# Optimization experiments

Hardware: AMD Instinct MI355X
Metric: run time of the kernel (lower is better)

The kernel has to match this reference:

```python
import jax, jax.numpy as jnp
import numpy as np

J = 21      # joints
C_ENC = 256 # encoding channels
C_IMG = 512 # img_feat channels
D = 64      # depth bins (hard-coded by view(-1, 256, 64))
EPS = 1e-5


def _soft_argmax_1d(h):
    # h: [B, J, L]
    p = jax.nn.softmax(h, axis=2)
    pos = jnp.arange(h.shape[2], dtype=h.dtype)
    return jnp.sum(p * pos, axis=2, keepdims=True)  # [B, J, 1]


def setup_inputs() -> dict:
    key = jax.random.key(0)
    ks = jax.random.split(key, 12)
    B, H, W = 16, 16, 16
    img_feat = jax.random.normal(ks[0], (B, C_IMG, H, W), dtype=jnp.float32)
    encoding = jax.random.normal(ks[1], (B, C_ENC, H, W), dtype=jnp.float32)
    # 1x1 conv weights stored as [out, in]
    wx = jax.random.normal(ks[2], (J, C_ENC), dtype=jnp.float32) * 0.02
    bx = jnp.zeros((J,), dtype=jnp.float32)
    wy = jax.random.normal(ks[3], (J, C_ENC), dtype=jnp.float32) * 0.02
    by = jnp.zeros((J,), dtype=jnp.float32)
    wz1 = jax.random.normal(ks[4], (C_ENC * D, C_IMG), dtype=jnp.float32) * 0.02
    bz1 = jnp.zeros((C_ENC * D,), dtype=jnp.float32)
    gamma = jax.random.uniform(ks[5], (C_ENC * D,), dtype=jnp.float32, minval=0.5, maxval=1.5)
    beta = jax.random.normal(ks[6], (C_ENC * D,), dtype=jnp.float32) * 0.1
    rmean = jax.random.normal(ks[7], (C_ENC * D,), dtype=jnp.float32) * 0.1
    rvar = jax.random.uniform(ks[8], (C_ENC * D,), dtype=jnp.float32, minval=0.5, maxval=1.5)
    wz2 = jax.random.normal(ks[9], (J, C_ENC), dtype=jnp.float32) * 0.02
    bz2 = jnp.zeros((J,), dtype=jnp.float32)
    return {"img_feat": img_feat, "encoding": encoding,
            "wx": wx, "bx": bx, "wy": wy, "by": by,
            "wz1": wz1, "bz1": bz1, "gamma": gamma, "beta": beta,
            "rmean": rmean, "rvar": rvar, "wz2": wz2, "bz2": bz2}


def reference(img_feat, encoding, wx, bx, wy, by, wz1, bz1, gamma, beta, rmean, rvar, wz2, bz2):
    B = encoding.shape[0]
    # x branch: mean over H (dim 2) -> [B, 256, W]
    feat_x = encoding.mean(axis=2)
    hx = jnp.einsum('jc,bcw->bjw', wx, feat_x) + bx[None, :, None]
    coord_x = _soft_argmax_1d(hx)
    # y branch: mean over W (dim 3) -> [B, 256, H]
    feat_y = encoding.mean(axis=3)
    hy = jnp.einsum('jc,bch->bjh', wy, feat_y) + by[None, :, None]
    coord_y = _soft_argmax_1d(hy)
    # z branch: global pool -> [B, 512] -> conv1x1 -> BN(eval) -> ReLU
    fz = img_feat.mean(axis=(2, 3))
    z = jnp.einsum('oc,bc->bo', wz1, fz) + bz1
    z = gamma * (z - rmean) * jax.lax.rsqrt(rvar + EPS) + beta
    z = jax.nn.relu(z)
    img_feat_z = z.reshape(B, C_ENC, D)  # [B, 256, 64]
    hz = jnp.einsum('jc,bcd->bjd', wz2, img_feat_z) + bz2[None, :, None]
    coord_z = _soft_argmax_1d(hz)
    joint_coord = jnp.concatenate([coord_x, coord_y, coord_z], axis=2)  # [B, J, 3]
    # fused replacement of the nested b/ch loop: broadcast multiply
    # [B,256,H,W,1] * [B,256,1,1,64] -> [B,256,H,W,64]
    img_feat_xyz = encoding[..., None] * img_feat_z[:, :, None, None, :]
    return joint_coord, img_feat_xyz
```

## Files before the change

### kernel.cpp

```cpp
#include <hip/hip_runtime.h>

#define EPS 1e-5f

typedef float f4 __attribute__((ext_vector_type(4)));

#define WS_FZ    0
#define WS_FX    8192
#define WS_FY    73728
#define WS_IMGZ  139264

__global__ __launch_bounds__(256) void k1_reduce(const float* __restrict__ img_feat,
                                                 const float* __restrict__ encoding,
                                                 float* __restrict__ ws) {
    int bid = blockIdx.x;
    if (bid < 2048) {
        int wave = (bid * 256 + (int)threadIdx.x) >> 6;
        int lane = threadIdx.x & 63;
        const f4* src = reinterpret_cast<const f4*>(img_feat + (size_t)wave * 256);
        f4 v = src[lane];
        float s = v.x + v.y + v.z + v.w;
        #pragma unroll
        for (int m = 32; m >= 1; m >>= 1) s += __shfl_xor(s, m, 64);
        if (lane == 0) ws[WS_FZ + wave] = s * (1.0f / 256.0f);
    } else {
        int t = (bid - 2048) * 256 + (int)threadIdx.x;
        if (t < 65536) {
            int w  = t & 15;
            int bc = t >> 4;
            const float* src = encoding + (size_t)bc * 256 + w;
            float s = 0.f;
            #pragma unroll
            for (int h = 0; h < 16; ++h) s += src[h * 16];
            ws[WS_FX + t] = s * (1.0f / 16.0f);
        } else {
            int u  = t - 65536;
            int h  = u & 15;
            int bc = u >> 4;
            const f4* src = reinterpret_cast<const f4*>(encoding + (size_t)bc * 256 + h * 16);
            f4 a = src[0], b = src[1], c = src[2], d = src[3];
            float s = (a.x + a.y + a.z + a.w) + (b.x + b.y + b.z + b.w)
                    + (c.x + c.y + c.z + c.w) + (d.x + d.y + d.z + d.w);
            ws[WS_FY + u] = s * (1.0f / 16.0f);
        }
    }
}

__global__ __launch_bounds__(256) void k2_zmlp(const float* __restrict__ wz1,
                                               const float* __restrict__ bz1,
                                               const float* __restrict__ gamma,
                                               const float* __restrict__ beta,
                                               const float* __restrict__ rmean,
                                               const float* __restrict__ rvar,
                                               float* __restrict__ ws) {
    __shared__ float fzl[16][516];
    int tid = threadIdx.x;
    #pragma unroll
    for (int i = 0; i < 32; ++i) {
        int idx = i * 256 + tid;
        fzl[idx >> 9][idx & 511] = ws[WS_FZ + idx];
    }
    __syncthreads();

    int o    = (blockIdx.x * 256 + tid) >> 6;
    int lane = tid & 63;
    int b    = lane & 15;
    int kg   = lane >> 4;
    const f4* wrow = reinterpret_cast<const f4*>(wz1 + (size_t)o * 512 + kg * 128);
    const f4* fr   = reinterpret_cast<const f4*>(&fzl[b][kg * 128]);
    float acc = 0.f;
    #pragma unroll
    for (int i = 0; i < 32; ++i) {
        f4 wv = wrow[i];
        f4 fv = fr[i];
        acc = fmaf(wv.x, fv.x, acc);
        acc = fmaf(wv.y, fv.y, acc);
        acc = fmaf(wv.z, fv.z, acc);
        acc = fmaf(wv.w, fv.w, acc);
    }
    acc += __shfl_xor(acc, 16, 64);
    acc += __shfl_xor(acc, 32, 64);
    if (lane < 16) {
        float z = acc + bz1[o];
        z = gamma[o] * (z - rmean[o]) * rsqrtf(rvar[o] + EPS) + beta[o];
        z = fmaxf(z, 0.f);
        ws[WS_IMGZ + (size_t)b * 16384 + o] = z;
    }
}

__global__ __launch_bounds__(128) void k3_coords(const float* __restrict__ wx,
                                                 const float* __restrict__ bx,
                                                 const float* __restrict__ wy,
                                                 const float* __restrict__ by,
                                                 const float* __restrict__ wz2,
                                                 const float* __restrict__ bz2,
                                                 const float* __restrict__ ws,
                                                 float* __restrict__ out_coord) {
    int bidx = blockIdx.x;
    int b = bidx / 21;
    int j = bidx - b * 21;
    int tid  = threadIdx.x;
    float* oj = out_coord + (size_t)b * 63 + j * 3;

    if (tid < 64) {
        int lane = tid;
        const float* imgz = ws + WS_IMGZ + (size_t)b * 16384;
        const float* wr   = wz2 + j * 256;
        float hz = bz2[j];
        #pragma unroll 8
        for (int c = 0; c < 256; ++c)
            hz = fmaf(wr[c], imgz[c * 64 + lane], hz);

        float m = hz;
        #pragma unroll
        for (int mk = 32; mk >= 1; mk >>= 1) m = fmaxf(m, __shfl_xor(m, mk, 64));
        float e = expf(hz - m);
        float s = e;
        float n = e * (float)lane;
        #pragma unroll
        for (int mk = 32; mk >= 1; mk >>= 1) {
            s += __shfl_xor(s, mk, 64);
            n += __shfl_xor(n, mk, 64);
        }
        if (lane == 0) oj[2] = n / s;
    } else if (tid < 96) {
        int lane = tid - 64;
        int w = lane & 15;
        const float* feat = (lane < 16) ? (ws + WS_FX + (size_t)b * 4096 + w)
                                        : (ws + WS_FY + (size_t)b * 4096 + w);
        const float* wrx  = (lane < 16) ? (wx + j * 256) : (wy + j * 256);
        float h = (lane < 16) ? bx[j] : by[j];
        #pragma unroll 8
        for (int c = 0; c < 256; ++c)
            h = fmaf(wrx[c], feat[c * 16], h);
        float mm = h;
        #pragma unroll
        for (int mk = 8; mk >= 1; mk >>= 1) mm = fmaxf(mm, __shfl_xor(mm, mk, 64));
        float ee = expf(h - mm);
        float ss = ee;
        float nn = ee * (float)w;
        #pragma unroll
        for (int mk = 8; mk >= 1; mk >>= 1) {
            ss += __shfl_xor(ss, mk, 64);
            nn += __shfl_xor(nn, mk, 64);
        }
        float cxy = nn / ss;
        if (lane == 0)  oj[0] = cxy;
        if (lane == 16) oj[1] = cxy;
    }
}

__global__ __launch_bounds__(256) void k4_bcast(const float* __restrict__ encoding,
                                                const float* __restrict__ ws,
                                                float* __restrict__ out_xyz) {
    unsigned int t = blockIdx.x * 256u + threadIdx.x;
    float e = encoding[t >> 4];
    const f4* imgz4 = reinterpret_cast<const f4*>(ws + WS_IMGZ);
    f4 zv = imgz4[((t >> 12) << 4) | (t & 15)];
    f4 r;
    r.x = e * zv.x; r.y = e * zv.y; r.z = e * zv.z; r.w = e * zv.w;
    __builtin_nontemporal_store(r, reinterpret_cast<f4*>(out_xyz) + t);
}

extern "C" void kernel_launch(void* const* d_in, const int* in_sizes, int n_in,
                              void* d_out, int out_size, void* d_ws, size_t ws_size,
                              hipStream_t stream) {
    const float* img_feat = (const float*)d_in[0];
    const float* encoding = (const float*)d_in[1];
    const float* wx   = (const float*)d_in[2];
    const float* bx   = (const float*)d_in[3];
    const float* wy   = (const float*)d_in[4];
    const float* by   = (const float*)d_in[5];
    const float* wz1  = (const float*)d_in[6];
    const float* bz1  = (const float*)d_in[7];
    const float* gamma= (const float*)d_in[8];
    const float* beta = (const float*)d_in[9];
    const float* rmean= (const float*)d_in[10];
    const float* rvar = (const float*)d_in[11];
    const float* wz2  = (const float*)d_in[12];
    const float* bz2  = (const float*)d_in[13];

    float* out = (float*)d_out;
    float* ws  = (float*)d_ws;

    k1_reduce<<<2560, 256, 0, stream>>>(img_feat, encoding, ws);
    k2_zmlp<<<4096, 256, 0, stream>>>(wz1, bz1, gamma, beta, rmean, rvar, ws);
    k3_coords<<<16 * 21, 128, 0, stream>>>(wx, bx, wy, by, wz2, bz2, ws, out);
    k4_bcast<<<65536, 256, 0, stream>>>(encoding, ws, out + 1008);
}
```

Measured before the change: 86.15 us.

## Regroup kernels so independent stages share launches and overlap

The encoding x/y mean reductions move out of the first kernel and into the z-MLP kernel as extra blocks. The coordinate kernel and the broadcast kernel merge into one launch, with the broadcast blocks placed after the coordinate blocks. This cuts one kernel launch and its tail/boundary bubble, letting the small coordinate work overlap the large broadcast store. In exchange, k2 blocks allocate the large shared array even when they only do reductions, and coord blocks now run with 256 threads where half sit idle.

```diff
diff --git a/kernel.cpp b/kernel.cpp
--- a/kernel.cpp
+++ b/kernel.cpp
@@ -9,21 +9,32 @@
 #define WS_FY    73728
 #define WS_IMGZ  139264
 
-__global__ __launch_bounds__(256) void k1_reduce(const float* __restrict__ img_feat,
-                                                 const float* __restrict__ encoding,
-                                                 float* __restrict__ ws) {
+__global__ __launch_bounds__(256) void k1_fz(const float* __restrict__ img_feat,
+                                             float* __restrict__ ws) {
+    int wave = (blockIdx.x * 256 + (int)threadIdx.x) >> 6;
+    int lane = threadIdx.x & 63;
+    const f4* src = reinterpret_cast<const f4*>(img_feat + (size_t)wave * 256);
+    f4 v = src[lane];
+    float s = v.x + v.y + v.z + v.w;
+    #pragma unroll
+    for (int m = 32; m >= 1; m >>= 1) s += __shfl_xor(s, m, 64);
+    if (lane == 0) ws[WS_FZ + wave] = s * (1.0f / 256.0f);
+}
+
+__global__ __launch_bounds__(256) void k2_zmlp(const float* __restrict__ wz1,
+                                               const float* __restrict__ bz1,
+                                               const float* __restrict__ gamma,
+                                               const float* __restrict__ beta,
+                                               const float* __restrict__ rmean,
+                                               const float* __restrict__ rvar,
+                                               const float* __restrict__ encoding,
+                                               float* __restrict__ ws) {
+    __shared__ float fzl[16][516];
+    int tid = threadIdx.x;
     int bid = blockIdx.x;
-    if (bid < 2048) {
-        int wave = (bid * 256 + (int)threadIdx.x) >> 6;
-        int lane = threadIdx.x & 63;
-        const f4* src = reinterpret_cast<const f4*>(img_feat + (size_t)wave * 256);
-        f4 v = src[lane];
-        float s = v.x + v.y + v.z + v.w;
-        #pragma unroll
-        for (int m = 32; m >= 1; m >>= 1) s += __shfl_xor(s, m, 64);
-        if (lane == 0) ws[WS_FZ + wave] = s * (1.0f / 256.0f);
-    } else {
-        int t = (bid - 2048) * 256 + (int)threadIdx.x;
+
+    if (bid >= 4096) {
+        int t = (bid - 4096) * 256 + tid;
         if (t < 65536) {
             int w  = t & 15;
             int bc = t >> 4;
@@ -42,18 +53,9 @@
                     + (c.x + c.y + c.z + c.w) + (d.x + d.y + d.z + d.w);
             ws[WS_FY + u] = s * (1.0f / 16.0f);
         }
+        return;
     }
-}
 
-__global__ __launch_bounds__(256) void k2_zmlp(const float* __restrict__ wz1,
-                                               const float* __restrict__ bz1,
-                                               const float* __restrict__ gamma,
-                                               const float* __restrict__ beta,
-                                               const float* __restrict__ rmean,
-                                               const float* __restrict__ rvar,
-                                               float* __restrict__ ws) {
-    __shared__ float fzl[16][516];
-    int tid = threadIdx.x;
     #pragma unroll
     for (int i = 0; i < 32; ++i) {
         int idx = i * 256 + tid;
@@ -61,7 +63,7 @@
     }
     __syncthreads();
 
-    int o    = (blockIdx.x * 256 + tid) >> 6;
+    int o    = (bid * 256 + tid) >> 6;
     int lane = tid & 63;
     int b    = lane & 15;
     int kg   = lane >> 4;
@@ -87,18 +89,32 @@
     }
 }
 
-__global__ __launch_bounds__(128) void k3_coords(const float* __restrict__ wx,
+__global__ __launch_bounds__(256) void k34_fused(const float* __restrict__ wx,
                                                  const float* __restrict__ bx,
                                                  const float* __restrict__ wy,
                                                  const float* __restrict__ by,
                                                  const float* __restrict__ wz2,
                                                  const float* __restrict__ bz2,
+                                                 const float* __restrict__ encoding,
                                                  const float* __restrict__ ws,
-                                                 float* __restrict__ out_coord) {
-    int bidx = blockIdx.x;
-    int b = bidx / 21;
-    int j = bidx - b * 21;
-    int tid  = threadIdx.x;
+                                                 float* __restrict__ out_coord,
+                                                 float* __restrict__ out_xyz) {
+    int bid = blockIdx.x;
+    int tid = threadIdx.x;
+
+    if (bid >= 336) {
+        unsigned int t = (unsigned int)(bid - 336) * 256u + tid;
+        float e = encoding[t >> 4];
+        const f4* imgz4 = reinterpret_cast<const f4*>(ws + WS_IMGZ);
+        f4 zv = imgz4[((t >> 12) << 4) | (t & 15)];
+        f4 r;
+        r.x = e * zv.x; r.y = e * zv.y; r.z = e * zv.z; r.w = e * zv.w;
+        __builtin_nontemporal_store(r, reinterpret_cast<f4*>(out_xyz) + t);
+        return;
+    }
+
+    int b = bid / 21;
+    int j = bid - b * 21;
     float* oj = out_coord + (size_t)b * 63 + j * 3;
 
     if (tid < 64) {
@@ -149,18 +165,6 @@
     }
 }
 
-__global__ __launch_bounds__(256) void k4_bcast(const float* __restrict__ encoding,
-                                                const float* __restrict__ ws,
-                                                float* __restrict__ out_xyz) {
-    unsigned int t = blockIdx.x * 256u + threadIdx.x;
-    float e = encoding[t >> 4];
-    const f4* imgz4 = reinterpret_cast<const f4*>(ws + WS_IMGZ);
-    f4 zv = imgz4[((t >> 12) << 4) | (t & 15)];
-    f4 r;
-    r.x = e * zv.x; r.y = e * zv.y; r.z = e * zv.z; r.w = e * zv.w;
-    __builtin_nontemporal_store(r, reinterpret_cast<f4*>(out_xyz) + t);
-}
-
 extern "C" void kernel_launch(void* const* d_in, const int* in_sizes, int n_in,
                               void* d_out, int out_size, void* d_ws, size_t ws_size,
                               hipStream_t stream) {
@@ -182,8 +186,9 @@
     float* out = (float*)d_out;
     float* ws  = (float*)d_ws;
 
-    k1_reduce<<<2560, 256, 0, stream>>>(img_feat, encoding, ws);
-    k2_zmlp<<<4096, 256, 0, stream>>>(wz1, bz1, gamma, beta, rmean, rvar, ws);
-    k3_coords<<<16 * 21, 128, 0, stream>>>(wx, bx, wy, by, wz2, bz2, ws, out);
-    k4_bcast<<<65536, 256, 0, stream>>>(encoding, ws, out + 1008);
+    k1_fz<<<2048, 256, 0, stream>>>(img_feat, ws);
+    k2_zmlp<<<4608, 256, 0, stream>>>(wz1, bz1, gamma, beta, rmean, rvar,
+                                      encoding, ws);
+    k34_fused<<<336 + 65536, 256, 0, stream>>>(wx, bx, wy, by, wz2, bz2,
+                                               encoding, ws, out, out + 1008);
 }
```

Measured after the change: 74.29 us, median of 2. -13.8%, faster.
